# Optimization experiments

Hardware: AMD Instinct MI355X
Metric: run time of the kernel (lower is better)

## Reference

```python
import jax, jax.numpy as jnp
import numpy as np

HIDDEN = 768
BATCH = 128


def setup_inputs() -> dict:
    key = jax.random.key(0)
    k_in, k_op = jax.random.split(key)
    inputs = jax.random.normal(k_in, (BATCH, HIDDEN, HIDDEN), dtype=jnp.float32)
    # nn.init.uniform_(operator, 0, 1)
    operator = jax.random.uniform(k_op, (HIDDEN, HIDDEN), dtype=jnp.float32)
    return {"inputs": inputs, "operator": operator}


def reference(inputs, operator):
    # Original: diag(operator @ inputs @ operator^T) then softmax over dim axis.
    # diag_i = sum_{j,k} operator[i,j] * inputs[b,j,k] * operator[i,k]
    # Compute first GEMM, then fuse the second matmul's diagonal as a dot-reduction.
    mm = jnp.einsum('ij,bjk->bik', operator, inputs)      # [b, d, d]
    diag = jnp.einsum('bik,ik->bi', mm, operator)          # [b, d]
    return jax.nn.softmax(diag, axis=1)
```

## Files before the change

kernel.cpp:

```cpp
#include <hip/hip_runtime.h>
#include <stdint.h>

#define HID 768
#define NB  128

typedef _Float16 half8    __attribute__((ext_vector_type(8)));
typedef __fp16   fp16x2   __attribute__((ext_vector_type(2)));
typedef float    float4_t __attribute__((ext_vector_type(4)));
typedef float    f32x16   __attribute__((ext_vector_type(16)));

#define OP_TILES (24 * 48)
#define OP_PLANE ((size_t)OP_TILES * 64 * 8)

__device__ __forceinline__ void convert8(const float4_t a, const float4_t b,
                                         half8& h, half8& l)
{
    fp16x2 h01 = __builtin_amdgcn_cvt_pkrtz(a[0], a[1]);
    fp16x2 h23 = __builtin_amdgcn_cvt_pkrtz(a[2], a[3]);
    fp16x2 h45 = __builtin_amdgcn_cvt_pkrtz(b[0], b[1]);
    fp16x2 h67 = __builtin_amdgcn_cvt_pkrtz(b[2], b[3]);
    fp16x2 l01 = __builtin_amdgcn_cvt_pkrtz(a[0] - (float)h01[0], a[1] - (float)h01[1]);
    fp16x2 l23 = __builtin_amdgcn_cvt_pkrtz(a[2] - (float)h23[0], a[3] - (float)h23[1]);
    fp16x2 l45 = __builtin_amdgcn_cvt_pkrtz(b[0] - (float)h45[0], b[1] - (float)h45[1]);
    fp16x2 l67 = __builtin_amdgcn_cvt_pkrtz(b[2] - (float)h67[0], b[3] - (float)h67[1]);
    h = (half8){(_Float16)h01[0], (_Float16)h01[1], (_Float16)h23[0], (_Float16)h23[1],
                (_Float16)h45[0], (_Float16)h45[1], (_Float16)h67[0], (_Float16)h67[1]};
    l = (half8){(_Float16)l01[0], (_Float16)l01[1], (_Float16)l23[0], (_Float16)l23[1],
                (_Float16)l45[0], (_Float16)l45[1], (_Float16)l67[0], (_Float16)l67[1]};
}

__global__ __launch_bounds__(256)
void split_op(const float* __restrict__ OP, _Float16* __restrict__ ws)
{
    const int g    = blockIdx.x * 256 + threadIdx.x;
    const int tile = g >> 6, lane = g & 63;
    const int i32t = tile / 48, k16 = tile % 48;
    const int i = i32t * 32 + (lane & 31);
    const int k = k16 * 16 + (lane >> 5) * 8;
    const float4_t a = *(const float4_t*)(OP + (size_t)i * HID + k);
    const float4_t b = *(const float4_t*)(OP + (size_t)i * HID + k + 4);
    half8 h, l;
    convert8(a, b, h, l);
    *(half8*)(ws + (size_t)(tile * 64 + lane) * 8) = h;
    *(half8*)(ws + OP_PLANE + (size_t)(tile * 64 + lane) * 8) = l;
}

__global__ __launch_bounds__(256, 3)
void diag_quad_kernel(const float* __restrict__ X, const float* __restrict__ OP,
                      const _Float16* __restrict__ opws, float* __restrict__ out)
{
    __shared__ __align__(16) float Abuf[2][4096];
    __shared__ float Dred[2][128];

    const int idx  = blockIdx.x;
    const int xcd  = idx & 7, slot = idx >> 3;
    const int b    = xcd * 16 + slot / 6;
    const int it   = slot % 6;
    const int i0   = it * 128;
    const float* Xb = X + (size_t)b * HID * HID;

    const int tid  = threadIdx.x;
    const int lane = tid & 63;
    const int wave = tid >> 6;
    const int wj   = wave & 1;
    const int wi   = wave >> 1;
    const int l5   = lane >> 5;
    const int m32  = lane & 31;

    const int srow = wave * 32 + m32;
    const int scol = l5 * 4;

    float p0 = 0.f, p1 = 0.f;

#define STAGE4(bufp, srcbase)                                                          \
    {                                                                                  \
        const float* _s = (srcbase);                                                   \
        _Pragma("unroll")                                                              \
        for (int _i = 0; _i < 4; ++_i)                                                 \
            __builtin_amdgcn_global_load_lds(                                          \
                (const __attribute__((address_space(1))) uint32_t*)(_s + _i * 8),      \
                (__attribute__((address_space(3))) uint32_t*)&(bufp)[(wave * 4 + _i) * 256], \
                16, 0, 0);                                                             \
    }

    STAGE4(Abuf[0], Xb + (size_t)srow * HID + scol);
    __syncthreads();

    f32x16 acc[2][2];
    int jt = 0, ks = 0;
    for (int t = 0; t < 144; ++t) {
        const int cur = t & 1;
        const int j0  = jt * 128;

        half8 bh[2][2], bl[2][2];
#pragma unroll
        for (int tj = 0; tj < 2; ++tj) {
            const int i32t = it * 4 + wi * 2 + tj;
#pragma unroll
            for (int kh = 0; kh < 2; ++kh) {
                const size_t o = ((size_t)(i32t * 48 + ks * 2 + kh)) * 512 + (size_t)lane * 8;
                bh[tj][kh] = *(const half8*)(opws + o);
                bl[tj][kh] = *(const half8*)(opws + OP_PLANE + o);
            }
        }

        int kn = ks + 1, jn = jt;
        if (kn == 24) { kn = 0; jn = jt + 1; }
        if (jn < 6)
            STAGE4(Abuf[cur ^ 1], Xb + (size_t)(jn * 128 + srow) * HID + kn * 32 + scol);

        if (ks == 0) {
#pragma unroll
            for (int ti = 0; ti < 2; ++ti)
#pragma unroll
                for (int tj = 0; tj < 2; ++tj)
#pragma unroll
                    for (int e = 0; e < 16; ++e) acc[ti][tj][e] = 0.f;
        }

        const float* Ab = Abuf[cur];
#pragma unroll
        for (int ti = 0; ti < 2; ++ti) {
            const int rt = wj * 2 + ti;
#pragma unroll
            for (int kh = 0; kh < 2; ++kh) {
                const int fb = ((rt * 2 + kh) * 128 + l5 * 64 + m32) * 4;
                const float4_t x0 = *(const float4_t*)&Ab[fb];
                const float4_t x1 = *(const float4_t*)&Ab[fb + 128];
                half8 ah, al;
                convert8(x0, x1, ah, al);
#pragma unroll
                for (int tj = 0; tj < 2; ++tj) {
                    acc[ti][tj] = __builtin_amdgcn_mfma_f32_32x32x16_f16(ah, bh[tj][kh], acc[ti][tj], 0, 0, 0);
                    acc[ti][tj] = __builtin_amdgcn_mfma_f32_32x32x16_f16(al, bh[tj][kh], acc[ti][tj], 0, 0, 0);
                    acc[ti][tj] = __builtin_amdgcn_mfma_f32_32x32x16_f16(ah, bl[tj][kh], acc[ti][tj], 0, 0, 0);
                }
            }
        }

        if (ks == 23) {
#pragma unroll
            for (int tj = 0; tj < 2; ++tj) {
                const int i_abs = i0 + wi * 64 + tj * 32 + m32;
                float s = 0.f;
#pragma unroll
                for (int ti = 0; ti < 2; ++ti) {
                    const int jb = j0 + wj * 64 + ti * 32 + l5 * 4;
#pragma unroll
                    for (int r2 = 0; r2 < 4; ++r2) {
                        const float4_t ov = *(const float4_t*)(OP + (size_t)i_abs * HID + jb + r2 * 8);
                        s += acc[ti][tj][r2 * 4 + 0] * ov[0]
                           + acc[ti][tj][r2 * 4 + 1] * ov[1]
                           + acc[ti][tj][r2 * 4 + 2] * ov[2]
                           + acc[ti][tj][r2 * 4 + 3] * ov[3];
                    }
                }
                if (tj == 0) p0 += s; else p1 += s;
            }
        }

        __syncthreads();
        ks = kn; jt = jn;
    }
#undef STAGE4

    p0 += __shfl_xor(p0, 32);
    p1 += __shfl_xor(p1, 32);
    if (lane < 32) {
        Dred[wj][wi * 64 + lane]      = p0;
        Dred[wj][wi * 64 + 32 + lane] = p1;
    }
    __syncthreads();
    if (tid < 128)
        out[(size_t)b * HID + i0 + tid] = Dred[0][tid] + Dred[1][tid];
}

__global__ __launch_bounds__(768)
void softmax_rows(float* __restrict__ out)
{
    const int row = blockIdx.x;
    const int t = threadIdx.x;
    const int wave = t >> 6, lane = t & 63;
    __shared__ float redm[12];
    __shared__ float reds[12];

    float v = out[(size_t)row * HID + t];

    float m = v;
#pragma unroll
    for (int o = 32; o >= 1; o >>= 1) m = fmaxf(m, __shfl_xor(m, o));
    if (lane == 0) redm[wave] = m;
    __syncthreads();
    if (t == 0) {
        float mm = redm[0];
        for (int w = 1; w < 12; ++w) mm = fmaxf(mm, redm[w]);
        redm[0] = mm;
    }
    __syncthreads();
    m = redm[0];

    const float e = expf(v - m);
    float s = e;
#pragma unroll
    for (int o = 32; o >= 1; o >>= 1) s += __shfl_xor(s, o);
    if (lane == 0) reds[wave] = s;
    __syncthreads();
    if (t == 0) {
        float ss = 0.f;
        for (int w = 0; w < 12; ++w) ss += reds[w];
        reds[0] = ss;
    }
    __syncthreads();
    out[(size_t)row * HID + t] = e / reds[0];
}

extern "C" void kernel_launch(void* const* d_in, const int* in_sizes, int n_in,
                              void* d_out, int out_size, void* d_ws, size_t ws_size,
                              hipStream_t stream)
{
    const float* X  = (const float*)d_in[0];
    const float* OP = (const float*)d_in[1];
    float* out = (float*)d_out;
    _Float16* opws = (_Float16*)d_ws;

    hipLaunchKernelGGL(split_op, dim3(OP_TILES / 4), dim3(256), 0, stream, OP, opws);
    hipLaunchKernelGGL(diag_quad_kernel, dim3(NB * 6), dim3(256), 0, stream, X, OP, opws, out);
    hipLaunchKernelGGL(softmax_rows, dim3(NB), dim3(768), 0, stream, out);
}
```

Before: 769.3 us.

## Triple-buffer LDS staging and register double-buffer operator fragments with manual waitcnt

Restructures the main GEMM loop into a deeper software pipeline. X tiles are staged two steps ahead into three LDS buffers. The fp16 hi/lo operator fragments are prefetched one step ahead into ping-pong register sets using inline-asm global loads. A manual s_waitcnt vmcnt(4) plus one raw s_barrier per step replaces the trailing __syncthreads, meant to hide global load latency behind MFMA work. In exchange it uses more LDS and registers, issues a few wasted wrap-around stage loads at the end, and depends on hand-counted vmcnt being correct.

Result: slower. 842.0 us (+9.4%).

```diff
diff --git a/kernel.cpp b/kernel.cpp
--- a/kernel.cpp
+++ b/kernel.cpp
@@ -45,11 +45,18 @@
     *(half8*)(ws + OP_PLANE + (size_t)(tile * 64 + lane) * 8) = l;
 }
 
+__device__ __forceinline__ half8 gld16(const _Float16* p)
+{
+    half8 d;
+    asm volatile("global_load_dwordx4 %0, %1, off" : "=&v"(d) : "v"(p));
+    return d;
+}
+
 __global__ __launch_bounds__(256, 3)
 void diag_quad_kernel(const float* __restrict__ X, const float* __restrict__ OP,
                       const _Float16* __restrict__ opws, float* __restrict__ out)
 {
-    __shared__ __align__(16) float Abuf[2][4096];
+    __shared__ __align__(16) float Abuf[3][4096];
     __shared__ float Dred[2][128];
 
     const int idx  = blockIdx.x;
@@ -69,99 +76,128 @@
 
     const int srow = wave * 32 + m32;
     const int scol = l5 * 4;
+    const int i32base = it * 4 + wi * 2;
 
     float p0 = 0.f, p1 = 0.f;
-
-#define STAGE4(bufp, srcbase)                                                          \
-    {                                                                                  \
-        const float* _s = (srcbase);                                                   \
+    half8 bhA[2][2], blA[2][2], bhB[2][2], blB[2][2];
+    f32x16 acc[2][2];
+
+#define STAGE4(bi, jtile, kstep)                                                       \
+    {                                                                                  \
+        const float* _s = Xb + (size_t)((jtile) * 128 + srow) * HID + (kstep) * 32 + scol; \
         _Pragma("unroll")                                                              \
         for (int _i = 0; _i < 4; ++_i)                                                 \
             __builtin_amdgcn_global_load_lds(                                          \
                 (const __attribute__((address_space(1))) uint32_t*)(_s + _i * 8),      \
-                (__attribute__((address_space(3))) uint32_t*)&(bufp)[(wave * 4 + _i) * 256], \
+                (__attribute__((address_space(3))) uint32_t*)(&Abuf[0][0] + (bi) * 4096 + (wave * 4 + _i) * 256), \
                 16, 0, 0);                                                             \
     }
 
-    STAGE4(Abuf[0], Xb + (size_t)srow * HID + scol);
-    __syncthreads();
-
-    f32x16 acc[2][2];
-    int jt = 0, ks = 0;
-    for (int t = 0; t < 144; ++t) {
-        const int cur = t & 1;
-        const int j0  = jt * 128;
-
-        half8 bh[2][2], bl[2][2];
-#pragma unroll
-        for (int tj = 0; tj < 2; ++tj) {
-            const int i32t = it * 4 + wi * 2 + tj;
-#pragma unroll
-            for (int kh = 0; kh < 2; ++kh) {
-                const size_t o = ((size_t)(i32t * 48 + ks * 2 + kh)) * 512 + (size_t)lane * 8;
-                bh[tj][kh] = *(const half8*)(opws + o);
-                bl[tj][kh] = *(const half8*)(opws + OP_PLANE + o);
-            }
-        }
-
-        int kn = ks + 1, jn = jt;
-        if (kn == 24) { kn = 0; jn = jt + 1; }
-        if (jn < 6)
-            STAGE4(Abuf[cur ^ 1], Xb + (size_t)(jn * 128 + srow) * HID + kn * 32 + scol);
-
-        if (ks == 0) {
-#pragma unroll
-            for (int ti = 0; ti < 2; ++ti)
-#pragma unroll
-                for (int tj = 0; tj < 2; ++tj)
-#pragma unroll
-                    for (int e = 0; e < 16; ++e) acc[ti][tj][e] = 0.f;
-        }
-
-        const float* Ab = Abuf[cur];
-#pragma unroll
-        for (int ti = 0; ti < 2; ++ti) {
-            const int rt = wj * 2 + ti;
-#pragma unroll
-            for (int kh = 0; kh < 2; ++kh) {
-                const int fb = ((rt * 2 + kh) * 128 + l5 * 64 + m32) * 4;
-                const float4_t x0 = *(const float4_t*)&Ab[fb];
-                const float4_t x1 = *(const float4_t*)&Ab[fb + 128];
-                half8 ah, al;
-                convert8(x0, x1, ah, al);
-#pragma unroll
-                for (int tj = 0; tj < 2; ++tj) {
-                    acc[ti][tj] = __builtin_amdgcn_mfma_f32_32x32x16_f16(ah, bh[tj][kh], acc[ti][tj], 0, 0, 0);
-                    acc[ti][tj] = __builtin_amdgcn_mfma_f32_32x32x16_f16(al, bh[tj][kh], acc[ti][tj], 0, 0, 0);
-                    acc[ti][tj] = __builtin_amdgcn_mfma_f32_32x32x16_f16(ah, bl[tj][kh], acc[ti][tj], 0, 0, 0);
-                }
-            }
-        }
-
-        if (ks == 23) {
-#pragma unroll
-            for (int tj = 0; tj < 2; ++tj) {
-                const int i_abs = i0 + wi * 64 + tj * 32 + m32;
-                float s = 0.f;
-#pragma unroll
-                for (int ti = 0; ti < 2; ++ti) {
-                    const int jb = j0 + wj * 64 + ti * 32 + l5 * 4;
-#pragma unroll
-                    for (int r2 = 0; r2 < 4; ++r2) {
-                        const float4_t ov = *(const float4_t*)(OP + (size_t)i_abs * HID + jb + r2 * 8);
-                        s += acc[ti][tj][r2 * 4 + 0] * ov[0]
-                           + acc[ti][tj][r2 * 4 + 1] * ov[1]
-                           + acc[ti][tj][r2 * 4 + 2] * ov[2]
-                           + acc[ti][tj][r2 * 4 + 3] * ov[3];
-                    }
-                }
-                if (tj == 0) p0 += s; else p1 += s;
-            }
-        }
-
-        __syncthreads();
-        ks = kn; jt = jn;
-    }
+#define LOADB(BH, BL, kss)                                                             \
+    {                                                                                  \
+        _Pragma("unroll")                                                              \
+        for (int _tj = 0; _tj < 2; ++_tj) {                                            \
+            _Pragma("unroll")                                                          \
+            for (int _kh = 0; _kh < 2; ++_kh) {                                        \
+                const size_t _o = ((size_t)((i32base + _tj) * 48 + (kss) * 2 + _kh)) * 512 \
+                                  + (size_t)lane * 8;                                  \
+                BH[_tj][_kh] = gld16(opws + _o);                                       \
+                BL[_tj][_kh] = gld16(opws + OP_PLANE + _o);                            \
+            }                                                                          \
+        }                                                                              \
+    }
+
+#define ZACC()                                                                         \
+    {                                                                                  \
+        _Pragma("unroll") for (int _a = 0; _a < 2; ++_a)                               \
+        _Pragma("unroll") for (int _b = 0; _b < 2; ++_b)                               \
+        _Pragma("unroll") for (int _e = 0; _e < 16; ++_e) acc[_a][_b][_e] = 0.f;       \
+    }
+
+#define COMPUTE(bi, BH, BL)                                                            \
+    {                                                                                  \
+        const float* Ab = &Abuf[0][0] + (bi) * 4096;                                   \
+        _Pragma("unroll")                                                              \
+        for (int _ti = 0; _ti < 2; ++_ti) {                                            \
+            const int _rt = wj * 2 + _ti;                                              \
+            _Pragma("unroll")                                                          \
+            for (int _kh = 0; _kh < 2; ++_kh) {                                        \
+                const int _fb = ((_rt * 2 + _kh) * 128 + l5 * 64 + m32) * 4;           \
+                const float4_t _x0 = *(const float4_t*)&Ab[_fb];                       \
+                const float4_t _x1 = *(const float4_t*)&Ab[_fb + 128];                 \
+                half8 _ah, _al;                                                        \
+                convert8(_x0, _x1, _ah, _al);                                          \
+                _Pragma("unroll")                                                      \
+                for (int _tj = 0; _tj < 2; ++_tj) {                                    \
+                    acc[_ti][_tj] = __builtin_amdgcn_mfma_f32_32x32x16_f16(_ah, BH[_tj][_kh], acc[_ti][_tj], 0, 0, 0); \
+                    acc[_ti][_tj] = __builtin_amdgcn_mfma_f32_32x32x16_f16(_al, BH[_tj][_kh], acc[_ti][_tj], 0, 0, 0); \
+                    acc[_ti][_tj] = __builtin_amdgcn_mfma_f32_32x32x16_f16(_ah, BL[_tj][_kh], acc[_ti][_tj], 0, 0, 0); \
+                }                                                                      \
+            }                                                                          \
+        }                                                                              \
+    }
+
+#define FOLD()                                                                         \
+    {                                                                                  \
+        const int _j0f = jt * 128;                                                     \
+        _Pragma("unroll")                                                              \
+        for (int _tj = 0; _tj < 2; ++_tj) {                                            \
+            const int _ia = i0 + wi * 64 + _tj * 32 + m32;                             \
+            float _s = 0.f;                                                            \
+            _Pragma("unroll")                                                          \
+            for (int _ti = 0; _ti < 2; ++_ti) {                                        \
+                const int _jb = _j0f + wj * 64 + _ti * 32 + l5 * 4;                    \
+                _Pragma("unroll")                                                      \
+                for (int _r2 = 0; _r2 < 4; ++_r2) {                                    \
+                    const float4_t _ov = *(const float4_t*)(OP + (size_t)_ia * HID + _jb + _r2 * 8); \
+                    _s += acc[_ti][_tj][_r2 * 4 + 0] * _ov[0]                          \
+                        + acc[_ti][_tj][_r2 * 4 + 1] * _ov[1]                          \
+                        + acc[_ti][_tj][_r2 * 4 + 2] * _ov[2]                          \
+                        + acc[_ti][_tj][_r2 * 4 + 3] * _ov[3];                         \
+                }                                                                      \
+            }                                                                          \
+            if (_tj == 0) p0 += _s; else p1 += _s;                                     \
+        }                                                                              \
+    }
+
+    int jt = 0, ks = 0, bufi = 0;
+    STAGE4(0, 0, 0);
+    __builtin_amdgcn_sched_barrier(0);
+    LOADB(bhA, blA, 0);
+    __builtin_amdgcn_sched_barrier(0);
+    STAGE4(1, 0, 1);
+    __builtin_amdgcn_sched_barrier(0);
+
+#define STEPBODY(BCH, BCL, BNH, BNL)                                                   \
+    {                                                                                  \
+        int _ksb = ks + 1; if (_ksb >= 24) _ksb = 0;              \
+        int _ksd = ks + 2, _jtd = jt;                                                  \
+        if (_ksd >= 24) { _ksd -= 24; _jtd = jt + 1; }                                 \
+        if (_jtd >= 6) _jtd = 0;                                \
+        int _bufd = bufi + 2; if (_bufd >= 3) _bufd -= 3;                              \
+        asm volatile("s_waitcnt vmcnt(4)" ::: "memory");         \
+        __builtin_amdgcn_s_barrier();                          \
+        __builtin_amdgcn_sched_barrier(0);                                             \
+        LOADB(BNH, BNL, _ksb);                                             \
+        __builtin_amdgcn_sched_barrier(0);                                             \
+        STAGE4(_bufd, _jtd, _ksd);                                       \
+        __builtin_amdgcn_sched_barrier(0);                                             \
+        if (ks == 0) ZACC();                                                           \
+        COMPUTE(bufi, BCH, BCL);                                                       \
+        if (ks == 23) FOLD();                                                          \
+        ++ks; if (ks == 24) { ks = 0; ++jt; }                                          \
+        ++bufi; if (bufi == 3) bufi = 0;                                               \
+    }
+
+    for (int th = 0; th < 72; ++th) {
+        STEPBODY(bhA, blA, bhB, blB);
+        STEPBODY(bhB, blB, bhA, blA);
+    }
+#undef STEPBODY
+#undef FOLD
+#undef COMPUTE
+#undef ZACC
+#undef LOADB
 #undef STAGE4
 
     p0 += __shfl_xor(p0, 32);
```
